# Kernel optimization log

Measured on AMD Instinct MI355X. Metric: run time of the kernel, lower is better.

Reference implementation:

```python
import jax, jax.numpy as jnp
from jax import lax
import numpy as np

S, B, T = 512, 256, 128


def setup_inputs() -> dict:
    key = jax.random.key(0)
    k1, k2, k3, k4 = jax.random.split(key, 4)
    emissions = jax.random.normal(k1, (S, B, T), dtype=jnp.float32)
    mask = jnp.ones((S, B), dtype=jnp.int32)  # all positions valid
    start_transitions = jax.random.normal(k2, (T,), dtype=jnp.float32)
    end_transitions = jax.random.normal(k3, (T,), dtype=jnp.float32)
    transitions = jax.random.normal(k4, (T, T), dtype=jnp.float32)
    return {
        "emissions": emissions,
        "mask": mask,
        "start_transitions": start_transitions,
        "end_transitions": end_transitions,
        "transitions": transitions,
    }


def reference(emissions, mask, start_transitions, end_transitions, transitions):
    """Viterbi decode. emissions: [S,B,T], mask: [S,B].
    Returns (best_tags [B,S] int32, best_path_score [B] float32)."""
    seq_len, batch, num_tags = emissions.shape
    maskb = mask.astype(bool)

    score0 = start_transitions[None, :] + emissions[0]  # [B,T]

    def fwd_step(score, inp):
        em_t, m_t = inp  # [B,T], [B]
        # [B, T_prev, T_next]
        ns = score[:, :, None] + transitions[None, :, :] + em_t[:, None, :]
        next_score = ns.max(axis=1)          # [B,T]
        idx = ns.argmax(axis=1)              # [B,T] best previous tag
        score = jnp.where(m_t[:, None], next_score, score)
        return score, idx

    final_score, history = lax.scan(fwd_step, score0, (emissions[1:], maskb[1:]))
    final_score = final_score + end_transitions[None, :]

    best_last = jnp.argmax(final_score, axis=1)   # [B] tag at last valid position
    best_score = jnp.max(final_score, axis=1)     # [B]

    barange = jnp.arange(batch)

    def back_step(tag, inp):
        hist_t, m_t = inp  # [B,T], [B]
        prev = hist_t[barange, tag]
        tag = jnp.where(m_t, prev, tag)  # only follow history inside the sequence
        return tag, tag

    # reverse scan over transitions t -> t+1 for t = S-2 .. 0; ys[t] = tag at time t
    _, tags_prefix = lax.scan(back_step, best_last, (history, maskb[1:]), reverse=True)
    tags = jnp.concatenate([tags_prefix, best_last[None, :]], axis=0)  # [S,B]
    return tags.T.astype(jnp.int32), best_score
```

## Files before the change

kernel.cpp:

```cpp
#include <hip/hip_runtime.h>

#define SLEN  512
#define BATCH 256
#define NTAGS 128
#define NTHR  512

__global__ __launch_bounds__(NTHR) void viterbi_kernel(
    const float* __restrict__ em,
    const int*   __restrict__ mask,
    const float* __restrict__ start_t,
    const float* __restrict__ end_t,
    const float* __restrict__ trans,
    float* __restrict__ out)
{
    const int b   = blockIdx.x;
    const int tid = threadIdx.x;
    const int j   = tid & (NTAGS - 1);
    const int h   = tid >> 7;

    __shared__ float sc[NTAGS];
    __shared__ float pmax[4][NTAGS];
    __shared__ int   pidx[4][NTAGS];
    __shared__ int   maskv[SLEN];
    __shared__ unsigned char hist[SLEN - 1][NTAGS];
    __shared__ unsigned char tagseq[SLEN];
    __shared__ float bestval_s;
    __shared__ int   bestj_s;

    float trcol[32];
#pragma unroll
    for (int k = 0; k < 32; ++k)
        trcol[k] = trans[(h * 32 + k) * NTAGS + j];

    for (int t = tid; t < SLEN; t += NTHR)
        maskv[t] = mask[t * BATCH + b];

    if (tid < NTAGS)
        sc[j] = start_t[j] + em[(size_t)b * NTAGS + j];
    __syncthreads();

    float em_next = em[(size_t)(1 * BATCH + b) * NTAGS + j];

    for (int t = 1; t < SLEN; ++t) {
        const float em_cur = em_next;
        if (t + 1 < SLEN)
            em_next = em[(size_t)((t + 1) * BATCH + b) * NTAGS + j];

        float best = -__builtin_inff();
        int   bidx = 0;
        const int base = h * 32;
#pragma unroll
        for (int k = 0; k < 32; ++k) {
            float c = (sc[base + k] + trcol[k]) + em_cur;
            if (c > best) { best = c; bidx = base + k; }
        }
        pmax[h][j] = best;
        pidx[h][j] = bidx;
        __syncthreads();

        if (h == 0) {
            float bv = pmax[0][j]; int bi = pidx[0][j];
#pragma unroll
            for (int hh = 1; hh < 4; ++hh) {
                float v = pmax[hh][j];
                if (v > bv) { bv = v; bi = pidx[hh][j]; }
            }
            hist[t - 1][j] = (unsigned char)bi;
            if (maskv[t]) sc[j] = bv;
        }
        __syncthreads();
    }

    if (tid < NTAGS) sc[j] = sc[j] + end_t[j];
    __syncthreads();

    if (tid < 64) {
        float v  = sc[tid]; int bj = tid;
        float v1 = sc[tid + 64];
        if (v1 > v) { v = v1; bj = tid + 64; }
#pragma unroll
        for (int off = 32; off > 0; off >>= 1) {
            float ov = __shfl_xor(v, off, 64);
            int   oj = __shfl_xor(bj, off, 64);
            if (ov > v || (ov == v && oj < bj)) { v = ov; bj = oj; }
        }
        if (tid == 0) { bestval_s = v; bestj_s = bj; }
    }
    __syncthreads();

    if (tid == 0) {
        int tag = bestj_s;
        tagseq[SLEN - 1] = (unsigned char)tag;
        for (int t = SLEN - 2; t >= 0; --t) {
            int prev = hist[t][tag];
            if (maskv[t + 1]) tag = prev;
            tagseq[t] = (unsigned char)tag;
        }
        out[BATCH * SLEN + b] = bestval_s;
    }
    __syncthreads();

    out[b * SLEN + tid] = (float)tagseq[tid];
}

extern "C" void kernel_launch(void* const* d_in, const int* in_sizes, int n_in,
                              void* d_out, int out_size, void* d_ws, size_t ws_size,
                              hipStream_t stream) {
    const float* em      = (const float*)d_in[0];
    const int*   mask    = (const int*)d_in[1];
    const float* start_t = (const float*)d_in[2];
    const float* end_t   = (const float*)d_in[3];
    const float* trans   = (const float*)d_in[4];
    float* out = (float*)d_out;

    viterbi_kernel<<<dim3(BATCH), dim3(NTHR), 0, stream>>>(
        em, mask, start_t, end_t, trans, out);
}
```

Measured before the change: 413.2 us.

## Reduce Viterbi argmax via DPP quad shuffles and parallelize backtrace in chunks

Each tag's 128 predecessors are now split across four adjacent lanes, which combine their partial argmax results with DPP quad permutes. This removes the second barrier and the shared partial-max arrays from each forward step. The score vector is double-buffered in padded shared memory and read as float4 vectors. The serial 511-step backtrace is replaced by a chunked scheme. It precomputes the exit tag of all 128 start tags for eight 64-step chunks, stitches the chunks serially, then runs the eight chunks in parallel. This adds extra shared-memory work and register pressure from the sv/bv/bi arrays.

```diff
diff --git a/kernel.cpp b/kernel.cpp
--- a/kernel.cpp
+++ b/kernel.cpp
@@ -4,6 +4,13 @@
 #define BATCH 256
 #define NTAGS 128
 #define NTHR  512
+
+__device__ __forceinline__ int dpp_qperm_b1(int x) {
+    return __builtin_amdgcn_update_dpp(0, x, 0xB1, 0xF, 0xF, true);
+}
+__device__ __forceinline__ int dpp_qperm_4e(int x) {
+    return __builtin_amdgcn_update_dpp(0, x, 0x4E, 0xF, 0xF, true);
+}
 
 __global__ __launch_bounds__(NTHR) void viterbi_kernel(
     const float* __restrict__ em,
@@ -15,14 +22,17 @@
 {
     const int b   = blockIdx.x;
     const int tid = threadIdx.x;
-    const int j   = tid & (NTAGS - 1);
-    const int h   = tid >> 7;
+    const int j   = tid >> 2;
+    const int h   = tid & 3;
+    const bool writer = (h == 0);
+    const int hbase = h << 5;
 
-    __shared__ float sc[NTAGS];
-    __shared__ float pmax[4][NTAGS];
-    __shared__ int   pidx[4][NTAGS];
+    __shared__ __align__(16) float scbuf[2][4 * 40];
+    __shared__ float fin[NTAGS];
     __shared__ int   maskv[SLEN];
     __shared__ unsigned char hist[SLEN - 1][NTAGS];
+    __shared__ unsigned char exitc[8][NTAGS];
+    __shared__ unsigned char st_tags[8];
     __shared__ unsigned char tagseq[SLEN];
     __shared__ float bestval_s;
     __shared__ int   bestj_s;
@@ -30,53 +40,85 @@
     float trcol[32];
 #pragma unroll
     for (int k = 0; k < 32; ++k)
-        trcol[k] = trans[(h * 32 + k) * NTAGS + j];
+        trcol[k] = trans[(hbase + k) * NTAGS + j];
 
     for (int t = tid; t < SLEN; t += NTHR)
         maskv[t] = mask[t * BATCH + b];
 
-    if (tid < NTAGS)
-        sc[j] = start_t[j] + em[(size_t)b * NTAGS + j];
+    float scj = 0.f;
+    if (writer) {
+        scj = start_t[j] + em[(size_t)b * NTAGS + j];
+        scbuf[0][j + (j >> 5) * 8] = scj;
+    }
     __syncthreads();
 
-    float em_next = em[(size_t)(1 * BATCH + b) * NTAGS + j];
+    const float* emp = em + (size_t)BATCH * NTAGS + (size_t)b * NTAGS + j;
+    float em_next = *emp;
 
+    int p = 0;
     for (int t = 1; t < SLEN; ++t) {
         const float em_cur = em_next;
-        if (t + 1 < SLEN)
-            em_next = em[(size_t)((t + 1) * BATCH + b) * NTAGS + j];
+        if (t + 1 < SLEN) { emp += BATCH * NTAGS; em_next = *emp; }
 
-        float best = -__builtin_inff();
-        int   bidx = 0;
-        const int base = h * 32;
+        float sv[32];
+        {
+            const float4* sp = (const float4*)&scbuf[p][h * 40];
 #pragma unroll
-        for (int k = 0; k < 32; ++k) {
-            float c = (sc[base + k] + trcol[k]) + em_cur;
-            if (c > best) { best = c; bidx = base + k; }
+            for (int r = 0; r < 8; ++r) {
+                float4 q = sp[r];
+                sv[4*r+0] = q.x; sv[4*r+1] = q.y; sv[4*r+2] = q.z; sv[4*r+3] = q.w;
+            }
         }
-        pmax[h][j] = best;
-        pidx[h][j] = bidx;
-        __syncthreads();
 
-        if (h == 0) {
-            float bv = pmax[0][j]; int bi = pidx[0][j];
+        float bv[16]; int bi[16];
 #pragma unroll
-            for (int hh = 1; hh < 4; ++hh) {
-                float v = pmax[hh][j];
-                if (v > bv) { bv = v; bi = pidx[hh][j]; }
+        for (int k = 0; k < 16; ++k) {
+            float ca = (sv[2*k]     + trcol[2*k])     + em_cur;
+            float cb = (sv[2*k + 1] + trcol[2*k + 1]) + em_cur;
+            bool tk = cb > ca;
+            bv[k] = tk ? cb : ca;
+            bi[k] = tk ? (2*k + 1) : (2*k);
+        }
+#pragma unroll
+        for (int w = 16; w > 1; w >>= 1) {
+#pragma unroll
+            for (int k = 0; k < (w >> 1); ++k) {
+                bool tk = bv[2*k + 1] > bv[2*k];
+                bv[k] = tk ? bv[2*k + 1] : bv[2*k];
+                bi[k] = tk ? bi[2*k + 1] : bi[2*k];
             }
-            hist[t - 1][j] = (unsigned char)bi;
-            if (maskv[t]) sc[j] = bv;
+        }
+
+        float v = bv[0];
+        int  gi = hbase + bi[0];
+        {
+            float vo = __int_as_float(dpp_qperm_b1(__float_as_int(v)));
+            int   io = dpp_qperm_b1(gi);
+            bool tk = vo > v;
+            v = tk ? vo : v; gi = tk ? io : gi;
+        }
+        {
+            float vo = __int_as_float(dpp_qperm_4e(__float_as_int(v)));
+            int   io = dpp_qperm_4e(gi);
+            bool tk = vo > v;
+            v = tk ? vo : v; gi = tk ? io : gi;
+        }
+
+        if (writer) {
+            hist[t - 1][j] = (unsigned char)gi;
+            scj = maskv[t] ? v : scj;
+            scbuf[p ^ 1][j + (j >> 5) * 8] = scj;
         }
         __syncthreads();
+        p ^= 1;
     }
 
-    if (tid < NTAGS) sc[j] = sc[j] + end_t[j];
+    if (tid < NTAGS) fin[tid] = scbuf[p][tid + (tid >> 5) * 8] + end_t[tid];
     __syncthreads();
 
     if (tid < 64) {
-        float v  = sc[tid]; int bj = tid;
-        float v1 = sc[tid + 64];
+        float v  = fin[tid]; int bj = tid;
+        float v1 = fin[tid + 64];
         if (v1 > v) { v = v1; bj = tid + 64; }
 #pragma unroll
         for (int off = 32; off > 0; off >>= 1) {
@@ -88,15 +130,46 @@
     }
     __syncthreads();
 
+    {
+        const int k  = tid & 127;
+        const int c0 = tid >> 7;
+        const int c1 = c0 + 4;
+        int tagA = k, tagB = k;
+        for (int u = 63; u >= 0; --u) {
+            const int sA = c0 * 64 + u;
+            const int sB = c1 * 64 + u;
+            if (sB <= SLEN - 2) {
+                int pv = hist[sB][tagB];
+                tagB = maskv[sB + 1] ? pv : tagB;
+            }
+            int pv = hist[sA][tagA];
+            tagA = maskv[sA + 1] ? pv : tagA;
+        }
+        exitc[c0][k] = (unsigned char)tagA;
+        exitc[c1][k] = (unsigned char)tagB;
+    }
+    __syncthreads();
+
     if (tid == 0) {
         int tag = bestj_s;
-        tagseq[SLEN - 1] = (unsigned char)tag;
-        for (int t = SLEN - 2; t >= 0; --t) {
-            int prev = hist[t][tag];
-            if (maskv[t + 1]) tag = prev;
-            tagseq[t] = (unsigned char)tag;
+        for (int c = 7; c >= 0; --c) {
+            st_tags[c] = (unsigned char)tag;
+            tag = exitc[c][tag];
         }
         out[BATCH * SLEN + b] = bestval_s;
+    }
+    __syncthreads();
+
+    if (tid < 8) {
+        const int c = tid;
+        int tag = st_tags[c];
+        if (c == 7) tagseq[SLEN - 1] = (unsigned char)tag;
+        const int shi = (c == 7) ? (SLEN - 2) : (c * 64 + 63);
+        for (int s = shi; s >= c * 64; --s) {
+            int pv = hist[s][tag];
+            tag = maskv[s + 1] ? pv : tag;
+            tagseq[s] = (unsigned char)tag;
+        }
     }
     __syncthreads();
 
```

Result: slower. 973.9 us (+135.7%).

## Parallelize Viterbi backtrace by chunks and vectorize forward max-reduction

Applied to the files above, without the earlier changes.

The serial 511-step backtrace on a single thread is replaced by a chunked scheme. All threads first compute, for every possible exit tag, where each 64-step chunk lands. One thread then chains the chunks together, and 8 threads replay the chunks in parallel to write the tags. The forward step now reads scores as float4 from shared memory and uses a tree-shaped max/argmax instead of a sequential chain, which shortens the dependency chain. The tree changes tie-breaking order slightly (it prefers the earlier index only within pairs), and the backtrace does more total work.

```diff
diff --git a/kernel.cpp b/kernel.cpp
--- a/kernel.cpp
+++ b/kernel.cpp
@@ -4,6 +4,9 @@
 #define BATCH 256
 #define NTAGS 128
 #define NTHR  512
+
+struct VI { float v; int i; };
+__device__ __forceinline__ VI vmax2(VI a, VI b) { return (b.v > a.v) ? b : a; }
 
 __global__ __launch_bounds__(NTHR) void viterbi_kernel(
     const float* __restrict__ em,
@@ -13,24 +16,32 @@
     const float* __restrict__ trans,
     float* __restrict__ out)
 {
-    const int b   = blockIdx.x;
-    const int tid = threadIdx.x;
-    const int j   = tid & (NTAGS - 1);
-    const int h   = tid >> 7;
+    const int b    = blockIdx.x;
+    const int tid  = threadIdx.x;
+    const int j    = tid & (NTAGS - 1);
+    const int h    = tid >> 7;
+    const int base = h << 5;
 
-    __shared__ float sc[NTAGS];
+    __shared__ __align__(16) float sc[NTAGS];
     __shared__ float pmax[4][NTAGS];
     __shared__ int   pidx[4][NTAGS];
     __shared__ int   maskv[SLEN];
     __shared__ unsigned char hist[SLEN - 1][NTAGS];
+    __shared__ unsigned char exitc[8][NTAGS];
+    __shared__ unsigned char st_tags[8];
     __shared__ unsigned char tagseq[SLEN];
     __shared__ float bestval_s;
     __shared__ int   bestj_s;
 
-    float trcol[32];
-#pragma unroll
-    for (int k = 0; k < 32; ++k)
-        trcol[k] = trans[(h * 32 + k) * NTAGS + j];
+    const float* trp = trans + (size_t)base * NTAGS + j;
+    const float t00 = trp[ 0*NTAGS], t01 = trp[ 1*NTAGS], t02 = trp[ 2*NTAGS], t03 = trp[ 3*NTAGS];
+    const float t04 = trp[ 4*NTAGS], t05 = trp[ 5*NTAGS], t06 = trp[ 6*NTAGS], t07 = trp[ 7*NTAGS];
+    const float t08 = trp[ 8*NTAGS], t09 = trp[ 9*NTAGS], t10 = trp[10*NTAGS], t11 = trp[11*NTAGS];
+    const float t12 = trp[12*NTAGS], t13 = trp[13*NTAGS], t14 = trp[14*NTAGS], t15 = trp[15*NTAGS];
+    const float t16 = trp[16*NTAGS], t17 = trp[17*NTAGS], t18 = trp[18*NTAGS], t19 = trp[19*NTAGS];
+    const float t20 = trp[20*NTAGS], t21 = trp[21*NTAGS], t22 = trp[22*NTAGS], t23 = trp[23*NTAGS];
+    const float t24 = trp[24*NTAGS], t25 = trp[25*NTAGS], t26 = trp[26*NTAGS], t27 = trp[27*NTAGS];
+    const float t28 = trp[28*NTAGS], t29 = trp[29*NTAGS], t30 = trp[30*NTAGS], t31 = trp[31*NTAGS];
 
     for (int t = tid; t < SLEN; t += NTHR)
         maskv[t] = mask[t * BATCH + b];
@@ -39,32 +50,66 @@
         sc[j] = start_t[j] + em[(size_t)b * NTAGS + j];
     __syncthreads();
 
-    float em_next = em[(size_t)(1 * BATCH + b) * NTAGS + j];
+    const float* emp = em + (size_t)BATCH * NTAGS + (size_t)b * NTAGS + j;
+    float em_next = *emp;
 
     for (int t = 1; t < SLEN; ++t) {
         const float em_cur = em_next;
-        if (t + 1 < SLEN)
-            em_next = em[(size_t)((t + 1) * BATCH + b) * NTAGS + j];
+        if (t + 1 < SLEN) { emp += BATCH * NTAGS; em_next = *emp; }
 
-        float best = -__builtin_inff();
-        int   bidx = 0;
-        const int base = h * 32;
-#pragma unroll
-        for (int k = 0; k < 32; ++k) {
-            float c = (sc[base + k] + trcol[k]) + em_cur;
-            if (c > best) { best = c; bidx = base + k; }
-        }
-        pmax[h][j] = best;
-        pidx[h][j] = bidx;
+        const float4* sq = (const float4*)&sc[base];
+        const float4 q0 = sq[0], q1 = sq[1], q2 = sq[2], q3 = sq[3];
+        const float4 q4 = sq[4], q5 = sq[5], q6 = sq[6], q7 = sq[7];
+
+        const float c00 = (q0.x + t00) + em_cur, c01 = (q0.y + t01) + em_cur;
+        const float c02 = (q0.z + t02) + em_cur, c03 = (q0.w + t03) + em_cur;
+        const float c04 = (q1.x + t04) + em_cur, c05 = (q1.y + t05) + em_cur;
+        const float c06 = (q1.z + t06) + em_cur, c07 = (q1.w + t07) + em_cur;
+        const float c08 = (q2.x + t08) + em_cur, c09 = (q2.y + t09) + em_cur;
+        const float c10 = (q2.z + t10) + em_cur, c11 = (q2.w + t11) + em_cur;
+        const float c12 = (q3.x + t12) + em_cur, c13 = (q3.y + t13) + em_cur;
+        const float c14 = (q3.z + t14) + em_cur, c15 = (q3.w + t15) + em_cur;
+        const float c16 = (q4.x + t16) + em_cur, c17 = (q4.y + t17) + em_cur;
+        const float c18 = (q4.z + t18) + em_cur, c19 = (q4.w + t19) + em_cur;
+        const float c20 = (q5.x + t20) + em_cur, c21 = (q5.y + t21) + em_cur;
+        const float c22 = (q5.z + t22) + em_cur, c23 = (q5.w + t23) + em_cur;
+        const float c24 = (q6.x + t24) + em_cur, c25 = (q6.y + t25) + em_cur;
+        const float c26 = (q6.z + t26) + em_cur, c27 = (q6.w + t27) + em_cur;
+        const float c28 = (q7.x + t28) + em_cur, c29 = (q7.y + t29) + em_cur;
+        const float c30 = (q7.z + t30) + em_cur, c31 = (q7.w + t31) + em_cur;
+
+        const VI m00 = vmax2(VI{c00, 0}, VI{c01, 1}),  m01 = vmax2(VI{c02, 2}, VI{c03, 3});
+        const VI m02 = vmax2(VI{c04, 4}, VI{c05, 5}),  m03 = vmax2(VI{c06, 6}, VI{c07, 7});
+        const VI m04 = vmax2(VI{c08, 8}, VI{c09, 9}),  m05 = vmax2(VI{c10,10}, VI{c11,11});
+        const VI m06 = vmax2(VI{c12,12}, VI{c13,13}),  m07 = vmax2(VI{c14,14}, VI{c15,15});
+        const VI m08 = vmax2(VI{c16,16}, VI{c17,17}),  m09 = vmax2(VI{c18,18}, VI{c19,19});
+        const VI m10 = vmax2(VI{c20,20}, VI{c21,21}),  m11 = vmax2(VI{c22,22}, VI{c23,23});
+        const VI m12 = vmax2(VI{c24,24}, VI{c25,25}),  m13 = vmax2(VI{c26,26}, VI{c27,27});
+        const VI m14 = vmax2(VI{c28,28}, VI{c29,29}),  m15 = vmax2(VI{c30,30}, VI{c31,31});
+
+        const VI n0 = vmax2(m00, m01), n1 = vmax2(m02, m03);
+        const VI n2 = vmax2(m04, m05), n3 = vmax2(m06, m07);
+        const VI n4 = vmax2(m08, m09), n5 = vmax2(m10, m11);
+        const VI n6 = vmax2(m12, m13), n7 = vmax2(m14, m15);
+
+        const VI o0 = vmax2(n0, n1), o1 = vmax2(n2, n3);
+        const VI o2 = vmax2(n4, n5), o3 = vmax2(n6, n7);
+
+        const VI p0 = vmax2(o0, o1), p1 = vmax2(o2, o3);
+        const VI r  = vmax2(p0, p1);
+
+        pmax[h][j] = r.v;
+        pidx[h][j] = base + r.i;
         __syncthreads();
 
-        if (h == 0) {
+        if (tid < NTAGS) {
             float bv = pmax[0][j]; int bi = pidx[0][j];
-#pragma unroll
-            for (int hh = 1; hh < 4; ++hh) {
-                float v = pmax[hh][j];
-                if (v > bv) { bv = v; bi = pidx[hh][j]; }
-            }
+            float v1 = pmax[1][j]; int i1 = pidx[1][j];
+            if (v1 > bv) { bv = v1; bi = i1; }
+            float v2 = pmax[2][j]; int i2 = pidx[2][j];
+            if (v2 > bv) { bv = v2; bi = i2; }
+            float v3 = pmax[3][j]; int i3 = pidx[3][j];
+            if (v3 > bv) { bv = v3; bi = i3; }
             hist[t - 1][j] = (unsigned char)bi;
             if (maskv[t]) sc[j] = bv;
         }
@@ -88,15 +133,46 @@
     }
     __syncthreads();
 
+    {
+        const int k  = tid & 127;
+        const int c0 = tid >> 7;
+        const int c1 = c0 + 4;
+        int tagA = k, tagB = k;
+        for (int u = 63; u >= 0; --u) {
+            const int sA = c0 * 64 + u;
+            const int sB = c1 * 64 + u;
+            if (sB <= SLEN - 2) {
+                int pv = hist[sB][tagB];
+                tagB = maskv[sB + 1] ? pv : tagB;
+            }
+            int pv = hist[sA][tagA];
+            tagA = maskv[sA + 1] ? pv : tagA;
+        }
+        exitc[c0][k] = (unsigned char)tagA;
+        exitc[c1][k] = (unsigned char)tagB;
+    }
+    __syncthreads();
+
     if (tid == 0) {
         int tag = bestj_s;
-        tagseq[SLEN - 1] = (unsigned char)tag;
-        for (int t = SLEN - 2; t >= 0; --t) {
-            int prev = hist[t][tag];
-            if (maskv[t + 1]) tag = prev;
-            tagseq[t] = (unsigned char)tag;
+        for (int c = 7; c >= 0; --c) {
+            st_tags[c] = (unsigned char)tag;
+            tag = exitc[c][tag];
         }
         out[BATCH * SLEN + b] = bestval_s;
+    }
+    __syncthreads();
+
+    if (tid < 8) {
+        const int c = tid;
+        int tag = st_tags[c];
+        if (c == 7) tagseq[SLEN - 1] = (unsigned char)tag;
+        const int shi = (c == 7) ? (SLEN - 2) : (c * 64 + 63);
+        for (int s = shi; s >= c * 64; --s) {
+            int pv = hist[s][tag];
+            tag = maskv[s + 1] ? pv : tag;
+            tagseq[s] = (unsigned char)tag;
+        }
     }
     __syncthreads();
 
```

New measurement: 416.0 us. Within noise of the previous version (+0.7%).
